# Kernel optimization log

Hardware: AMD Instinct MI355X
Metric: run time of the kernel (lower is better)

## Reference

```python
import jax, jax.numpy as jnp
import numpy as np

B, S, D, H = 1, 2048, 1024, 16
HD = D // H
FF = 4 * D
EPS_LN = 1e-5
EPS_ATTN = 1e-6


def _layernorm(x, g, b):
    mu = jnp.mean(x, axis=-1, keepdims=True)
    var = jnp.mean(jnp.square(x - mu), axis=-1, keepdims=True)
    return (x - mu) * jax.lax.rsqrt(var + EPS_LN) * g + b


def setup_inputs() -> dict:
    key = jax.random.key(0)
    ks = jax.random.split(key, 12)
    w = lambda k, shape: (jax.random.normal(k, shape, jnp.float32) * 0.02)
    return {
        "x": jax.random.normal(ks[0], (B, S, D), jnp.float32),
        "Wq": w(ks[1], (D, D)), "bq": jnp.zeros((D,), jnp.float32),
        "Wk": w(ks[2], (D, D)), "bk": jnp.zeros((D,), jnp.float32),
        "Wv": w(ks[3], (D, D)), "bv": jnp.zeros((D,), jnp.float32),
        "Wo": w(ks[4], (D, D)), "bo": jnp.zeros((D,), jnp.float32),
        "W1": w(ks[5], (FF, D)), "bb1": jnp.zeros((FF,), jnp.float32),
        "W2": w(ks[6], (D, FF)), "bb2": jnp.zeros((D,), jnp.float32),
        "g1": jnp.ones((D,), jnp.float32), "be1": jnp.zeros((D,), jnp.float32),
        "g2": jnp.ones((D,), jnp.float32), "be2": jnp.zeros((D,), jnp.float32),
    }


def reference(x, Wq, bq, Wk, bk, Wv, bv, Wo, bo, W1, bb1, W2, bb2, g1, be1, g2, be2):
    # --- pre-norm causal linear attention ---
    h = _layernorm(x, g1, be1)                     # (B,S,D)
    def heads(t):
        return t.reshape(B, S, H, HD).transpose(0, 2, 1, 3)  # (B,H,S,hd)
    q = heads(h @ Wq.T + bq)
    k = heads(h @ Wk.T + bk)
    v = heads(h @ Wv.T + bv)
    # feature map phi(x) = elu(x) + 1 (strictly positive)
    q = jax.nn.elu(q) + 1.0
    k = jax.nn.elu(k) + 1.0
    # causal cumulative state: S_t = sum_{i<=t} k_i v_i^T ; z_t = sum_{i<=t} k_i
    kv = jnp.cumsum(jnp.einsum("bhsd,bhse->bhsde", k, v), axis=2)  # (B,H,S,hd,hd)
    z = jnp.cumsum(k, axis=2)                                       # (B,H,S,hd)
    num = jnp.einsum("bhsd,bhsde->bhse", q, kv)                    # (B,H,S,hd)
    den = jnp.einsum("bhsd,bhsd->bhs", q, z) + EPS_ATTN
    attn = (num / den[..., None]).transpose(0, 2, 1, 3).reshape(B, S, D)
    attn = attn @ Wo.T + bo
    x = x + attn
    # --- FFN (GELU exact, matching torch nn.GELU default) ---
    h2 = _layernorm(x, g2, be2)
    ff = jax.nn.gelu(h2 @ W1.T + bb1, approximate=False) @ W2.T + bb2
    return x + ff
```

## Files before the change

### kernel.cpp

```cpp
#include <hip/hip_runtime.h>
#include <hip/hip_bf16.h>
#include <math.h>

constexpr int S  = 2048;
constexpr int D  = 1024;
constexpr int H  = 16;
constexpr int HD = 64;
constexpr int FF = 4096;
constexpr int NC  = 32;
constexpr int CHK = 64;
constexpr int QS  = 3 * D;

typedef __attribute__((ext_vector_type(8))) short bf16x8;
typedef __attribute__((ext_vector_type(4))) float f32x4;

__device__ inline unsigned short f2bf(float f) {
    unsigned int u = __float_as_uint(f);
    u = (u + 0x7FFFu + ((u >> 16) & 1u)) >> 16;
    return (unsigned short)u;
}

constexpr int DD4 = D * D / 4;
constexpr int FD4 = FF * D / 4;
constexpr int CVT_TOTAL4 = 4 * DD4 + 2 * FD4;

__global__ __launch_bounds__(256) void cvt6(const float* __restrict__ Wq,
                                            const float* __restrict__ Wk,
                                            const float* __restrict__ Wv,
                                            const float* __restrict__ Wo,
                                            const float* __restrict__ W1,
                                            const float* __restrict__ W2,
                                            unsigned short* __restrict__ Wqkvb,
                                            unsigned short* __restrict__ Wob,
                                            unsigned short* __restrict__ W1b,
                                            unsigned short* __restrict__ W2b) {
    int i = blockIdx.x * 256 + threadIdx.x;
    if (i >= CVT_TOTAL4) return;
    const float* s;
    unsigned short* dp;
    if (i < DD4)                 { s = Wq + (size_t)i * 4;               dp = Wqkvb + (size_t)i * 4; }
    else if (i < 2 * DD4)        { s = Wk + (size_t)(i - DD4) * 4;       dp = Wqkvb + (size_t)i * 4; }
    else if (i < 3 * DD4)        { s = Wv + (size_t)(i - 2 * DD4) * 4;   dp = Wqkvb + (size_t)i * 4; }
    else if (i < 4 * DD4)        { s = Wo + (size_t)(i - 3 * DD4) * 4;   dp = Wob + (size_t)(i - 3 * DD4) * 4; }
    else if (i < 4 * DD4 + FD4)  { s = W1 + (size_t)(i - 4 * DD4) * 4;   dp = W1b + (size_t)(i - 4 * DD4) * 4; }
    else                         { s = W2 + (size_t)(i - 4 * DD4 - FD4) * 4; dp = W2b + (size_t)(i - 4 * DD4 - FD4) * 4; }
    float4 v = *(const float4*)s;
    ushort4 o = { f2bf(v.x), f2bf(v.y), f2bf(v.z), f2bf(v.w) };
    *(ushort4*)dp = o;
}

__global__ __launch_bounds__(256) void layernorm_bf16(const float* __restrict__ x,
                                                      const float* __restrict__ g,
                                                      const float* __restrict__ b,
                                                      unsigned short* __restrict__ out) {
    const int row = blockIdx.x, tid = threadIdx.x;
    float4 v = ((const float4*)(x + (size_t)row * D))[tid];
    float s  = v.x + v.y + v.z + v.w;
    float ss = v.x*v.x + v.y*v.y + v.z*v.z + v.w*v.w;
    #pragma unroll
    for (int off = 32; off > 0; off >>= 1) {
        s  += __shfl_down(s, off);
        ss += __shfl_down(ss, off);
    }
    __shared__ float sw[4], ssw[4];
    if ((tid & 63) == 0) { sw[tid >> 6] = s; ssw[tid >> 6] = ss; }
    __syncthreads();
    s  = sw[0] + sw[1] + sw[2] + sw[3];
    ss = ssw[0] + ssw[1] + ssw[2] + ssw[3];
    const float mu = s * (1.0f / D);
    const float rs = rsqrtf(ss * (1.0f / D) - mu * mu + 1e-5f);
    float4 gv = ((const float4*)g)[tid];
    float4 bv = ((const float4*)b)[tid];
    ushort4 o = { f2bf((v.x - mu) * rs * gv.x + bv.x),
                  f2bf((v.y - mu) * rs * gv.y + bv.y),
                  f2bf((v.z - mu) * rs * gv.z + bv.z),
                  f2bf((v.w - mu) * rs * gv.w + bv.w) };
    ((ushort4*)(out + (size_t)row * D))[tid] = o;
}

template <int KS>
__global__ __launch_bounds__(256) void reduce_ln(const float* __restrict__ part,
                                                 const float* __restrict__ bias,
                                                 const float* __restrict__ res,
                                                 float* __restrict__ x2,
                                                 const float* __restrict__ g,
                                                 const float* __restrict__ b,
                                                 unsigned short* __restrict__ out) {
    const int row = blockIdx.x, tid = threadIdx.x;
    const size_t i4 = (size_t)row * 256 + tid;
    float4 a = ((const float4*)part)[i4];
    #pragma unroll
    for (int z = 1; z < KS; ++z) {
        float4 p = ((const float4*)part)[(size_t)z * S * 256 + i4];
        a.x += p.x; a.y += p.y; a.z += p.z; a.w += p.w;
    }
    float4 bi = ((const float4*)bias)[tid];
    float4 r  = ((const float4*)res)[i4];
    a.x += bi.x + r.x; a.y += bi.y + r.y; a.z += bi.z + r.z; a.w += bi.w + r.w;
    ((float4*)x2)[i4] = a;
    float s  = a.x + a.y + a.z + a.w;
    float ss = a.x*a.x + a.y*a.y + a.z*a.z + a.w*a.w;
    #pragma unroll
    for (int off = 32; off > 0; off >>= 1) {
        s  += __shfl_down(s, off);
        ss += __shfl_down(ss, off);
    }
    __shared__ float sw[4], ssw[4];
    if ((tid & 63) == 0) { sw[tid >> 6] = s; ssw[tid >> 6] = ss; }
    __syncthreads();
    s  = sw[0] + sw[1] + sw[2] + sw[3];
    ss = ssw[0] + ssw[1] + ssw[2] + ssw[3];
    const float mu = s * (1.0f / D);
    const float rs = rsqrtf(ss * (1.0f / D) - mu * mu + 1e-5f);
    float4 gv = ((const float4*)g)[tid];
    float4 bv = ((const float4*)b)[tid];
    ushort4 o = { f2bf((a.x - mu) * rs * gv.x + bv.x),
                  f2bf((a.y - mu) * rs * gv.y + bv.y),
                  f2bf((a.z - mu) * rs * gv.z + bv.z),
                  f2bf((a.w - mu) * rs * gv.w + bv.w) };
    ((ushort4*)(out + (size_t)row * D))[tid] = o;
}

template <int KS>
__global__ __launch_bounds__(256) void reduce_bias_res(const float* __restrict__ part,
                                                       const float* __restrict__ bias,
                                                       const float* __restrict__ res,
                                                       float* __restrict__ out,
                                                       int N4, int total4) {
    int i = blockIdx.x * 256 + threadIdx.x;
    if (i >= total4) return;
    float4 a = ((const float4*)part)[i];
    #pragma unroll
    for (int z = 1; z < KS; ++z) {
        float4 p = ((const float4*)part)[(size_t)z * total4 + i];
        a.x += p.x; a.y += p.y; a.z += p.z; a.w += p.w;
    }
    float4 b = ((const float4*)bias)[i % N4];
    float4 r = ((const float4*)res)[i];
    a.x += b.x + r.x; a.y += b.y + r.y; a.z += b.z + r.z; a.w += b.w + r.w;
    ((float4*)out)[i] = a;
}

enum { EPI_F32 = 0, EPI_QKV = 1, EPI_GELU_BF16 = 2, EPI_PART = 3 };

template <int EPI>
__global__ __launch_bounds__(256, 2) void gemm_bt(const unsigned short* __restrict__ A,
                                                  const unsigned short* __restrict__ W,
                                                  const float* __restrict__ bias,
                                                  const float* __restrict__ bias2,
                                                  const float* __restrict__ bias3,
                                                  void* __restrict__ outp,
                                                  int M, int N, int K, int kSplit) {
    __shared__ unsigned short As[2][128 * 64];
    __shared__ unsigned short Bs[2][128 * 64];
    const int tid  = threadIdx.x;
    const int tileM = blockIdx.x * 128;
    const int tileN = blockIdx.y * 128;
    const int w    = tid >> 6, lane = tid & 63;
    const int wm   = (w >> 1) * 64, wn = (w & 1) * 64;
    const int lr   = lane & 15, lk = lane >> 4;
    const int sw   = (lr >> 1) & 7;
    const int kLen   = K / kSplit;
    const int kStart = blockIdx.z * kLen;
    const int kEnd   = kStart + kLen;

    f32x4 acc[4][4];
    #pragma unroll
    for (int i = 0; i < 4; ++i)
        #pragma unroll
        for (int j = 0; j < 4; ++j) acc[i][j] = (f32x4)(0.0f);

    auto stage = [&](int buf, int k0) {
        #pragma unroll
        for (int p = 0; p < 4; ++p) {
            const int c   = p * 256 + tid;
            const int row = c >> 3;
            const int kc  = (c & 7) ^ ((row >> 1) & 7);
            __builtin_amdgcn_global_load_lds(
                (const __attribute__((address_space(1))) unsigned int*)
                    (A + (size_t)(tileM + row) * K + k0 + kc * 8),
                (__attribute__((address_space(3))) unsigned int*)&As[buf][c * 8],
                16, 0, 0);
            __builtin_amdgcn_global_load_lds(
                (const __attribute__((address_space(1))) unsigned int*)
                    (W + (size_t)(tileN + row) * K + k0 + kc * 8),
                (__attribute__((address_space(3))) unsigned int*)&Bs[buf][c * 8],
                16, 0, 0);
        }
    };

    stage(0, kStart);
    __syncthreads();
    int buf = 0;
    for (int k0 = kStart; k0 < kEnd; k0 += 64) {
        if (k0 + 64 < kEnd) stage(buf ^ 1, k0 + 64);
        #pragma unroll
        for (int kk = 0; kk < 2; ++kk) {
            bf16x8 af[4], bfv[4];
            #pragma unroll
            for (int i = 0; i < 4; ++i) {
                const int row = wm + i * 16 + lr;
                af[i] = *(const bf16x8*)&As[buf][row * 64 + ((((kk << 2) | lk) ^ sw) << 3)];
            }
            #pragma unroll
            for (int j = 0; j < 4; ++j) {
                const int row = wn + j * 16 + lr;
                bfv[j] = *(const bf16x8*)&Bs[buf][row * 64 + ((((kk << 2) | lk) ^ sw) << 3)];
            }
            #pragma unroll
            for (int i = 0; i < 4; ++i)
                #pragma unroll
                for (int j = 0; j < 4; ++j)
                    acc[i][j] = __builtin_amdgcn_mfma_f32_16x16x32_bf16(af[i], bfv[j], acc[i][j], 0, 0, 0);
        }
        __syncthreads();
        buf ^= 1;
    }

    #pragma unroll
    for (int i = 0; i < 4; ++i) {
        const int rbase = tileM + wm + i * 16 + lk * 4;
        #pragma unroll
        for (int j = 0; j < 4; ++j) {
            const int col = tileN + wn + j * 16 + lr;
            #pragma unroll
            for (int r = 0; r < 4; ++r) {
                const int row = rbase + r;
                const size_t off = (size_t)row * N + col;
                float v = acc[i][j][r];
                if constexpr (EPI == EPI_PART) {
                    ((float*)outp)[(size_t)blockIdx.z * (size_t)M * (size_t)N + off] = v;
                } else if constexpr (EPI == EPI_QKV) {
                    float bc = (col < D) ? bias[col] : ((col < 2 * D) ? bias2[col - D] : bias3[col - 2 * D]);
                    v += bc;
                    if (col < 2 * D) v = v > 0.0f ? v + 1.0f : __expf(v);
                    ((float*)outp)[off] = v;
                } else if constexpr (EPI == EPI_GELU_BF16) {
                    v += bias[col];
                    float gl = 0.5f * v * (1.0f + erff(v * 0.70710678118654752f));
                    ((unsigned short*)outp)[off] = f2bf(gl);
                } else {
                    v += bias[col];
                    ((float*)outp)[off] = v;
                }
            }
        }
    }
}

__global__ __launch_bounds__(256) void attn_chunk_sums(const float* __restrict__ qkv,
                                                       float* __restrict__ KVc,
                                                       float* __restrict__ Zc) {
    const int c = blockIdx.x, h = blockIdx.y, tid = threadIdx.x;
    __shared__ float Kc[CHK * HD], Vc[CHK * HD];
    const int s0 = c * CHK;
    #pragma unroll
    for (int p = 0; p < 4; ++p) {
        int cc = p * 256 + tid;
        int t = cc >> 4, dp = (cc & 15) * 4;
        *(float4*)&Kc[t * HD + dp] = *(const float4*)(qkv + (size_t)(s0 + t) * QS + D     + h * HD + dp);
        *(float4*)&Vc[t * HD + dp] = *(const float4*)(qkv + (size_t)(s0 + t) * QS + 2 * D + h * HD + dp);
    }
    __syncthreads();
    const int d = tid >> 2, e0 = (tid & 3) * 16;
    float acc[16];
    #pragma unroll
    for (int j = 0; j < 16; ++j) acc[j] = 0.0f;
    float zacc = 0.0f;
    for (int t = 0; t < CHK; ++t) {
        float kv = Kc[t * HD + d];
        zacc += kv;
        #pragma unroll
        for (int j = 0; j < 16; ++j) acc[j] += kv * Vc[t * HD + e0 + j];
    }
    float* op = KVc + ((size_t)(h * NC + c) * HD + d) * HD + e0;
    #pragma unroll
    for (int j = 0; j < 16; ++j) op[j] = acc[j];
    if ((tid & 3) == 0) Zc[(size_t)(h * NC + c) * HD + d] = zacc;
}

__global__ __launch_bounds__(256) void attn_prefix(float* __restrict__ KVc,
                                                   float* __restrict__ Zc) {
    const int h = blockIdx.y;
    const int elem = blockIdx.x * 256 + threadIdx.x;
    size_t base = (size_t)h * NC * (HD * HD) + elem;
    float run = 0.0f;
    for (int c = 0; c < NC; ++c) {
        float t = KVc[base + (size_t)c * (HD * HD)];
        KVc[base + (size_t)c * (HD * HD)] = run;
        run += t;
    }
    if (blockIdx.x == 0 && threadIdx.x < HD) {
        size_t zb = (size_t)h * NC * HD + threadIdx.x;
        float zr = 0.0f;
        for (int c = 0; c < NC; ++c) {
            float t = Zc[zb + (size_t)c * HD];
            Zc[zb + (size_t)c * HD] = zr;
            zr += t;
        }
    }
}

__global__ __launch_bounds__(256) void attn_out(const float* __restrict__ qkv,
                                                const float* __restrict__ KVpre,
                                                const float* __restrict__ Zpre,
                                                unsigned short* __restrict__ attn) {
    const int c = blockIdx.x, h = blockIdx.y, tid = threadIdx.x;
    __shared__ float Qc[CHK * HD], KVs[CHK * HD], Pre[HD * HD], Sc[CHK * CHK];
    __shared__ float zp[HD], den[CHK];
    const int s0 = c * CHK;
    #pragma unroll
    for (int p = 0; p < 4; ++p) {
        int cc = p * 256 + tid;
        int t = cc >> 4, dp = (cc & 15) * 4;
        *(float4*)&Qc[t * HD + dp]  = *(const float4*)(qkv + (size_t)(s0 + t) * QS +     h * HD + dp);
        *(float4*)&KVs[t * HD + dp] = *(const float4*)(qkv + (size_t)(s0 + t) * QS + D + h * HD + dp);
        ((float4*)Pre)[cc] = *(const float4*)(KVpre + (size_t)(h * NC + c) * (HD * HD) + cc * 4);
    }
    if (tid < HD) zp[tid] = Zpre[(size_t)(h * NC + c) * HD + tid];
    __syncthreads();

    const int tt = tid >> 2, i0 = (tid & 3) * 16;
    for (int i = i0; i < i0 + 16; ++i) {
        float sv = 0.0f;
        for (int d2 = 0; d2 < HD; ++d2) sv += Qc[tt * HD + d2] * KVs[i * HD + d2];
        Sc[tt * CHK + i] = (i <= tt) ? sv : 0.0f;
    }
    __syncthreads();

    if (tid < CHK) {
        float dv = 1e-6f;
        for (int d2 = 0; d2 < HD; ++d2) dv += Qc[tid * HD + d2] * zp[d2];
        for (int i = 0; i < CHK; ++i) dv += Sc[tid * CHK + i];
        den[tid] = dv;
    }
    #pragma unroll
    for (int p = 0; p < 4; ++p) {
        int cc = p * 256 + tid;
        int t = cc >> 4, dp = (cc & 15) * 4;
        *(float4*)&KVs[t * HD + dp] = *(const float4*)(qkv + (size_t)(s0 + t) * QS + 2 * D + h * HD + dp);
    }
    __syncthreads();

    float o[16];
    #pragma unroll
    for (int j = 0; j < 16; ++j) o[j] = 0.0f;
    for (int d2 = 0; d2 < HD; ++d2) {
        float qv = Qc[tt * HD + d2];
        float sv = Sc[tt * CHK + d2];
        #pragma unroll
        for (int j = 0; j < 16; ++j)
            o[j] += qv * Pre[d2 * HD + i0 + j] + sv * KVs[d2 * HD + i0 + j];
    }
    const float inv = 1.0f / den[tt];
    unsigned short* op = attn + (size_t)(s0 + tt) * D + h * HD + i0;
    #pragma unroll
    for (int j0 = 0; j0 < 16; j0 += 4) {
        ushort4 ov = { f2bf(o[j0] * inv), f2bf(o[j0 + 1] * inv),
                       f2bf(o[j0 + 2] * inv), f2bf(o[j0 + 3] * inv) };
        *(ushort4*)(op + j0) = ov;
    }
}

extern "C" void kernel_launch(void* const* d_in, const int* in_sizes, int n_in,
                              void* d_out, int out_size, void* d_ws, size_t ws_size,
                              hipStream_t stream) {
    const float* x   = (const float*)d_in[0];
    const float* Wq  = (const float*)d_in[1];
    const float* bq  = (const float*)d_in[2];
    const float* Wk  = (const float*)d_in[3];
    const float* bk  = (const float*)d_in[4];
    const float* Wv  = (const float*)d_in[5];
    const float* bv  = (const float*)d_in[6];
    const float* Wo  = (const float*)d_in[7];
    const float* bo  = (const float*)d_in[8];
    const float* W1  = (const float*)d_in[9];
    const float* b1  = (const float*)d_in[10];
    const float* W2  = (const float*)d_in[11];
    const float* b2  = (const float*)d_in[12];
    const float* g1  = (const float*)d_in[13];
    const float* be1 = (const float*)d_in[14];
    const float* g2  = (const float*)d_in[15];
    const float* be2 = (const float*)d_in[16];
    float* out = (float*)d_out;

    char* wsp = (char*)d_ws;
    auto alloc = [&](size_t bytes) {
        char* p = wsp;
        wsp += (bytes + 255) & ~(size_t)255;
        return p;
    };
    unsigned short* h1   = (unsigned short*)alloc((size_t)S * D * 2);
    unsigned short* attn = (unsigned short*)alloc((size_t)S * D * 2);
    unsigned short* gbuf = (unsigned short*)alloc((size_t)S * FF * 2);
    float* x2   = (float*)alloc((size_t)S * D * 4);
    unsigned short* Wqkvb = (unsigned short*)alloc((size_t)3 * D * D * 2);
    unsigned short* Wob   = (unsigned short*)alloc((size_t)D * D * 2);
    unsigned short* W1b   = (unsigned short*)alloc((size_t)FF * D * 2);
    unsigned short* W2b   = (unsigned short*)alloc((size_t)D * FF * 2);
    float* KVc  = (float*)alloc((size_t)H * NC * HD * HD * 4);
    float* Zc   = (float*)alloc((size_t)H * NC * HD * 4);
    char* uni = (char*)alloc((size_t)32 * 1024 * 1024);
    float* qkv   = (float*)uni;
    float* parts = (float*)uni;

    cvt6<<<(CVT_TOTAL4 + 255) / 256, 256, 0, stream>>>(Wq, Wk, Wv, Wo, W1, W2,
                                                       Wqkvb, Wob, W1b, W2b);

    layernorm_bf16<<<S, 256, 0, stream>>>(x, g1, be1, h1);

    gemm_bt<EPI_QKV><<<dim3(S / 128, 3 * D / 128, 1), 256, 0, stream>>>(
        h1, Wqkvb, bq, bk, bv, qkv, S, 3 * D, D, 1);

    attn_chunk_sums<<<dim3(NC, H), 256, 0, stream>>>(qkv, KVc, Zc);
    attn_prefix<<<dim3(16, H), 256, 0, stream>>>(KVc, Zc);
    attn_out<<<dim3(NC, H), 256, 0, stream>>>(qkv, KVc, Zc, attn);

    gemm_bt<EPI_PART><<<dim3(S / 128, D / 128, 4), 256, 0, stream>>>(
        attn, Wob, nullptr, nullptr, nullptr, parts, S, D, D, 4);
    reduce_ln<4><<<S, 256, 0, stream>>>(parts, bo, x, x2, g2, be2, h1);

    gemm_bt<EPI_GELU_BF16><<<dim3(S / 128, FF / 128, 1), 256, 0, stream>>>(
        h1, W1b, b1, nullptr, nullptr, gbuf, S, FF, D, 1);

    gemm_bt<EPI_PART><<<dim3(S / 128, D / 128, 4), 256, 0, stream>>>(
        gbuf, W2b, nullptr, nullptr, nullptr, parts, S, D, FF, 4);
    reduce_bias_res<4><<<(S * D / 4 + 255) / 256, 256, 0, stream>>>(
        parts, b2, x2, out, D / 4, S * D / 4);
}
```

Measured before the change: 280.3 us.

## Replace split-K partial buffers with atomic accumulation into pre-initialized outputs

The split-K GEMMs for the output projection and the second FFN layer now atomically add their partial results into destination buffers instead of writing four partial slabs and reducing them in separate kernels. The destinations are pre-initialized with residual plus bias: x2 inside a merged prep kernel that also does the weight conversion and the first layernorm, and out inside the second layernorm kernel. This removes the partial-buffer writes and reads and two reduction passes, and folds two early launches into one. In exchange it adds float atomic traffic with nondeterministic summation order, and the epilogue's scalar atomics may be slower than plain stores.

```diff
diff --git a/kernel.cpp b/kernel.cpp
--- a/kernel.cpp
+++ b/kernel.cpp
@@ -23,8 +23,10 @@
 constexpr int DD4 = D * D / 4;
 constexpr int FD4 = FF * D / 4;
 constexpr int CVT_TOTAL4 = 4 * DD4 + 2 * FD4;
-
-__global__ __launch_bounds__(256) void cvt6(const float* __restrict__ Wq,
+constexpr int NB_CVT  = CVT_TOTAL4 / 256;
+constexpr int NB_INIT = S * D / 4 / 256;
+
+__global__ __launch_bounds__(256) void prep(const float* __restrict__ Wq,
                                             const float* __restrict__ Wk,
                                             const float* __restrict__ Wv,
                                             const float* __restrict__ Wo,
@@ -33,71 +35,72 @@
                                             unsigned short* __restrict__ Wqkvb,
                                             unsigned short* __restrict__ Wob,
                                             unsigned short* __restrict__ W1b,
-                                            unsigned short* __restrict__ W2b) {
-    int i = blockIdx.x * 256 + threadIdx.x;
-    if (i >= CVT_TOTAL4) return;
-    const float* s;
-    unsigned short* dp;
-    if (i < DD4)                 { s = Wq + (size_t)i * 4;               dp = Wqkvb + (size_t)i * 4; }
-    else if (i < 2 * DD4)        { s = Wk + (size_t)(i - DD4) * 4;       dp = Wqkvb + (size_t)i * 4; }
-    else if (i < 3 * DD4)        { s = Wv + (size_t)(i - 2 * DD4) * 4;   dp = Wqkvb + (size_t)i * 4; }
-    else if (i < 4 * DD4)        { s = Wo + (size_t)(i - 3 * DD4) * 4;   dp = Wob + (size_t)(i - 3 * DD4) * 4; }
-    else if (i < 4 * DD4 + FD4)  { s = W1 + (size_t)(i - 4 * DD4) * 4;   dp = W1b + (size_t)(i - 4 * DD4) * 4; }
-    else                         { s = W2 + (size_t)(i - 4 * DD4 - FD4) * 4; dp = W2b + (size_t)(i - 4 * DD4 - FD4) * 4; }
-    float4 v = *(const float4*)s;
-    ushort4 o = { f2bf(v.x), f2bf(v.y), f2bf(v.z), f2bf(v.w) };
-    *(ushort4*)dp = o;
-}
-
-__global__ __launch_bounds__(256) void layernorm_bf16(const float* __restrict__ x,
-                                                      const float* __restrict__ g,
-                                                      const float* __restrict__ b,
-                                                      unsigned short* __restrict__ out) {
-    const int row = blockIdx.x, tid = threadIdx.x;
-    float4 v = ((const float4*)(x + (size_t)row * D))[tid];
-    float s  = v.x + v.y + v.z + v.w;
-    float ss = v.x*v.x + v.y*v.y + v.z*v.z + v.w*v.w;
-    #pragma unroll
-    for (int off = 32; off > 0; off >>= 1) {
-        s  += __shfl_down(s, off);
-        ss += __shfl_down(ss, off);
-    }
-    __shared__ float sw[4], ssw[4];
-    if ((tid & 63) == 0) { sw[tid >> 6] = s; ssw[tid >> 6] = ss; }
-    __syncthreads();
-    s  = sw[0] + sw[1] + sw[2] + sw[3];
-    ss = ssw[0] + ssw[1] + ssw[2] + ssw[3];
-    const float mu = s * (1.0f / D);
-    const float rs = rsqrtf(ss * (1.0f / D) - mu * mu + 1e-5f);
-    float4 gv = ((const float4*)g)[tid];
-    float4 bv = ((const float4*)b)[tid];
-    ushort4 o = { f2bf((v.x - mu) * rs * gv.x + bv.x),
-                  f2bf((v.y - mu) * rs * gv.y + bv.y),
-                  f2bf((v.z - mu) * rs * gv.z + bv.z),
-                  f2bf((v.w - mu) * rs * gv.w + bv.w) };
-    ((ushort4*)(out + (size_t)row * D))[tid] = o;
-}
-
-template <int KS>
-__global__ __launch_bounds__(256) void reduce_ln(const float* __restrict__ part,
-                                                 const float* __restrict__ bias,
-                                                 const float* __restrict__ res,
-                                                 float* __restrict__ x2,
-                                                 const float* __restrict__ g,
-                                                 const float* __restrict__ b,
-                                                 unsigned short* __restrict__ out) {
+                                            unsigned short* __restrict__ W2b,
+                                            const float* __restrict__ x,
+                                            const float* __restrict__ g1,
+                                            const float* __restrict__ be1,
+                                            unsigned short* __restrict__ h1,
+                                            const float* __restrict__ bo,
+                                            float* __restrict__ x2) {
+    const int b = blockIdx.x, tid = threadIdx.x;
+    if (b < NB_CVT) {
+        int i = b * 256 + tid;
+        const float* s;
+        unsigned short* dp;
+        if (i < DD4)                 { s = Wq + (size_t)i * 4;               dp = Wqkvb + (size_t)i * 4; }
+        else if (i < 2 * DD4)        { s = Wk + (size_t)(i - DD4) * 4;       dp = Wqkvb + (size_t)i * 4; }
+        else if (i < 3 * DD4)        { s = Wv + (size_t)(i - 2 * DD4) * 4;   dp = Wqkvb + (size_t)i * 4; }
+        else if (i < 4 * DD4)        { s = Wo + (size_t)(i - 3 * DD4) * 4;   dp = Wob + (size_t)(i - 3 * DD4) * 4; }
+        else if (i < 4 * DD4 + FD4)  { s = W1 + (size_t)(i - 4 * DD4) * 4;   dp = W1b + (size_t)(i - 4 * DD4) * 4; }
+        else                         { s = W2 + (size_t)(i - 4 * DD4 - FD4) * 4; dp = W2b + (size_t)(i - 4 * DD4 - FD4) * 4; }
+        float4 v = *(const float4*)s;
+        ushort4 o = { f2bf(v.x), f2bf(v.y), f2bf(v.z), f2bf(v.w) };
+        *(ushort4*)dp = o;
+    } else if (b < NB_CVT + S) {
+        const int row = b - NB_CVT;
+        float4 v = ((const float4*)(x + (size_t)row * D))[tid];
+        float s  = v.x + v.y + v.z + v.w;
+        float ss = v.x*v.x + v.y*v.y + v.z*v.z + v.w*v.w;
+        #pragma unroll
+        for (int off = 32; off > 0; off >>= 1) {
+            s  += __shfl_down(s, off);
+            ss += __shfl_down(ss, off);
+        }
+        __shared__ float sw[4], ssw[4];
+        if ((tid & 63) == 0) { sw[tid >> 6] = s; ssw[tid >> 6] = ss; }
+        __syncthreads();
+        s  = sw[0] + sw[1] + sw[2] + sw[3];
+        ss = ssw[0] + ssw[1] + ssw[2] + ssw[3];
+        const float mu = s * (1.0f / D);
+        const float rs = rsqrtf(ss * (1.0f / D) - mu * mu + 1e-5f);
+        float4 gv = ((const float4*)g1)[tid];
+        float4 bv = ((const float4*)be1)[tid];
+        ushort4 o = { f2bf((v.x - mu) * rs * gv.x + bv.x),
+                      f2bf((v.y - mu) * rs * gv.y + bv.y),
+                      f2bf((v.z - mu) * rs * gv.z + bv.z),
+                      f2bf((v.w - mu) * rs * gv.w + bv.w) };
+        ((ushort4*)(h1 + (size_t)row * D))[tid] = o;
+    } else {
+        const int i = (b - NB_CVT - S) * 256 + tid;
+        float4 v = ((const float4*)x)[i];
+        float4 bb = ((const float4*)bo)[i & 255];
+        v.x += bb.x; v.y += bb.y; v.z += bb.z; v.w += bb.w;
+        ((float4*)x2)[i] = v;
+    }
+}
+
+__global__ __launch_bounds__(256) void ln2_init(const float* __restrict__ x2,
+                                                const float* __restrict__ g,
+                                                const float* __restrict__ b,
+                                                const float* __restrict__ b2,
+                                                unsigned short* __restrict__ hout,
+                                                float* __restrict__ out) {
     const int row = blockIdx.x, tid = threadIdx.x;
     const size_t i4 = (size_t)row * 256 + tid;
-    float4 a = ((const float4*)part)[i4];
-    #pragma unroll
-    for (int z = 1; z < KS; ++z) {
-        float4 p = ((const float4*)part)[(size_t)z * S * 256 + i4];
-        a.x += p.x; a.y += p.y; a.z += p.z; a.w += p.w;
-    }
-    float4 bi = ((const float4*)bias)[tid];
-    float4 r  = ((const float4*)res)[i4];
-    a.x += bi.x + r.x; a.y += bi.y + r.y; a.z += bi.z + r.z; a.w += bi.w + r.w;
-    ((float4*)x2)[i4] = a;
+    float4 a = ((const float4*)x2)[i4];
+    float4 b2v = ((const float4*)b2)[tid];
+    float4 ov = { a.x + b2v.x, a.y + b2v.y, a.z + b2v.z, a.w + b2v.w };
+    ((float4*)out)[i4] = ov;
     float s  = a.x + a.y + a.z + a.w;
     float ss = a.x*a.x + a.y*a.y + a.z*a.z + a.w*a.w;
     #pragma unroll
@@ -118,30 +121,10 @@
                   f2bf((a.y - mu) * rs * gv.y + bv.y),
                   f2bf((a.z - mu) * rs * gv.z + bv.z),
                   f2bf((a.w - mu) * rs * gv.w + bv.w) };
-    ((ushort4*)(out + (size_t)row * D))[tid] = o;
-}
-
-template <int KS>
-__global__ __launch_bounds__(256) void reduce_bias_res(const float* __restrict__ part,
-                                                       const float* __restrict__ bias,
-                                                       const float* __restrict__ res,
-                                                       float* __restrict__ out,
-                                                       int N4, int total4) {
-    int i = blockIdx.x * 256 + threadIdx.x;
-    if (i >= total4) return;
-    float4 a = ((const float4*)part)[i];
-    #pragma unroll
-    for (int z = 1; z < KS; ++z) {
-        float4 p = ((const float4*)part)[(size_t)z * total4 + i];
-        a.x += p.x; a.y += p.y; a.z += p.z; a.w += p.w;
-    }
-    float4 b = ((const float4*)bias)[i % N4];
-    float4 r = ((const float4*)res)[i];
-    a.x += b.x + r.x; a.y += b.y + r.y; a.z += b.z + r.z; a.w += b.w + r.w;
-    ((float4*)out)[i] = a;
-}
-
-enum { EPI_F32 = 0, EPI_QKV = 1, EPI_GELU_BF16 = 2, EPI_PART = 3 };
+    ((ushort4*)(hout + (size_t)row * D))[tid] = o;
+}
+
+enum { EPI_F32 = 0, EPI_QKV = 1, EPI_GELU_BF16 = 2, EPI_ATOM = 3 };
 
 template <int EPI>
 __global__ __launch_bounds__(256, 2) void gemm_bt(const unsigned short* __restrict__ A,
@@ -228,8 +211,8 @@
                 const int row = rbase + r;
                 const size_t off = (size_t)row * N + col;
                 float v = acc[i][j][r];
-                if constexpr (EPI == EPI_PART) {
-                    ((float*)outp)[(size_t)blockIdx.z * (size_t)M * (size_t)N + off] = v;
+                if constexpr (EPI == EPI_ATOM) {
+                    atomicAdd(&((float*)outp)[off], v);
                 } else if constexpr (EPI == EPI_QKV) {
                     float bc = (col < D) ? bias[col] : ((col < 2 * D) ? bias2[col - D] : bias3[col - 2 * D]);
                     v += bc;
@@ -400,14 +383,11 @@
     unsigned short* W2b   = (unsigned short*)alloc((size_t)D * FF * 2);
     float* KVc  = (float*)alloc((size_t)H * NC * HD * HD * 4);
     float* Zc   = (float*)alloc((size_t)H * NC * HD * 4);
-    char* uni = (char*)alloc((size_t)32 * 1024 * 1024);
-    float* qkv   = (float*)uni;
-    float* parts = (float*)uni;
-
-    cvt6<<<(CVT_TOTAL4 + 255) / 256, 256, 0, stream>>>(Wq, Wk, Wv, Wo, W1, W2,
-                                                       Wqkvb, Wob, W1b, W2b);
-
-    layernorm_bf16<<<S, 256, 0, stream>>>(x, g1, be1, h1);
+    float* qkv  = (float*)alloc((size_t)S * QS * 4);
+
+    prep<<<NB_CVT + S + NB_INIT, 256, 0, stream>>>(Wq, Wk, Wv, Wo, W1, W2,
+                                                   Wqkvb, Wob, W1b, W2b,
+                                                   x, g1, be1, h1, bo, x2);
 
     gemm_bt<EPI_QKV><<<dim3(S / 128, 3 * D / 128, 1), 256, 0, stream>>>(
         h1, Wqkvb, bq, bk, bv, qkv, S, 3 * D, D, 1);
@@ -416,15 +396,14 @@
     attn_prefix<<<dim3(16, H), 256, 0, stream>>>(KVc, Zc);
     attn_out<<<dim3(NC, H), 256, 0, stream>>>(qkv, KVc, Zc, attn);
 
-    gemm_bt<EPI_PART><<<dim3(S / 128, D / 128, 4), 256, 0, stream>>>(
-        attn, Wob, nullptr, nullptr, nullptr, parts, S, D, D, 4);
-    reduce_ln<4><<<S, 256, 0, stream>>>(parts, bo, x, x2, g2, be2, h1);
+    gemm_bt<EPI_ATOM><<<dim3(S / 128, D / 128, 4), 256, 0, stream>>>(
+        attn, Wob, nullptr, nullptr, nullptr, x2, S, D, D, 4);
+
+    ln2_init<<<S, 256, 0, stream>>>(x2, g2, be2, b2, h1, out);
 
     gemm_bt<EPI_GELU_BF16><<<dim3(S / 128, FF / 128, 1), 256, 0, stream>>>(
         h1, W1b, b1, nullptr, nullptr, gbuf, S, FF, D, 1);
 
-    gemm_bt<EPI_PART><<<dim3(S / 128, D / 128, 4), 256, 0, stream>>>(
-        gbuf, W2b, nullptr, nullptr, nullptr, parts, S, D, FF, 4);
-    reduce_bias_res<4><<<(S * D / 4 + 255) / 256, 256, 0, stream>>>(
-        parts, b2, x2, out, D / 4, S * D / 4);
-}
+    gemm_bt<EPI_ATOM><<<dim3(S / 128, D / 128, 4), 256, 0, stream>>>(
+        gbuf, W2b, nullptr, nullptr, nullptr, out, S, D, FF, 4);
+}
```

After: 307.1 us. +9.5%, slower.

## Shrink GEMM M-tile to 64, merge weight conversion with first layernorm

Applied to the files above, without the earlier changes.

The GEMM tile changes from 128x128 to 64x128, which halves the A staging and accumulators and raises the occupancy hint to 3 blocks per CU. Grids and split-K factors are adjusted to match: the Wo GEMM goes from 4 to 2 splits with a matching reduce, and the W2 GEMM keeps 4 splits. The weight bf16 conversion and the first layernorm are merged into one launch to save a kernel launch. The aim is more blocks to fill the many CUs and less partial-sum traffic, at the cost of lower per-block arithmetic intensity, since more B tiles must be reloaded.

```diff
diff --git a/kernel.cpp b/kernel.cpp
--- a/kernel.cpp
+++ b/kernel.cpp
@@ -23,8 +23,9 @@
 constexpr int DD4 = D * D / 4;
 constexpr int FD4 = FF * D / 4;
 constexpr int CVT_TOTAL4 = 4 * DD4 + 2 * FD4;
-
-__global__ __launch_bounds__(256) void cvt6(const float* __restrict__ Wq,
+constexpr int NB_CVT  = CVT_TOTAL4 / 256;
+
+__global__ __launch_bounds__(256) void prep(const float* __restrict__ Wq,
                                             const float* __restrict__ Wk,
                                             const float* __restrict__ Wv,
                                             const float* __restrict__ Wo,
@@ -33,49 +34,50 @@
                                             unsigned short* __restrict__ Wqkvb,
                                             unsigned short* __restrict__ Wob,
                                             unsigned short* __restrict__ W1b,
-                                            unsigned short* __restrict__ W2b) {
-    int i = blockIdx.x * 256 + threadIdx.x;
-    if (i >= CVT_TOTAL4) return;
-    const float* s;
-    unsigned short* dp;
-    if (i < DD4)                 { s = Wq + (size_t)i * 4;               dp = Wqkvb + (size_t)i * 4; }
-    else if (i < 2 * DD4)        { s = Wk + (size_t)(i - DD4) * 4;       dp = Wqkvb + (size_t)i * 4; }
-    else if (i < 3 * DD4)        { s = Wv + (size_t)(i - 2 * DD4) * 4;   dp = Wqkvb + (size_t)i * 4; }
-    else if (i < 4 * DD4)        { s = Wo + (size_t)(i - 3 * DD4) * 4;   dp = Wob + (size_t)(i - 3 * DD4) * 4; }
-    else if (i < 4 * DD4 + FD4)  { s = W1 + (size_t)(i - 4 * DD4) * 4;   dp = W1b + (size_t)(i - 4 * DD4) * 4; }
-    else                         { s = W2 + (size_t)(i - 4 * DD4 - FD4) * 4; dp = W2b + (size_t)(i - 4 * DD4 - FD4) * 4; }
-    float4 v = *(const float4*)s;
-    ushort4 o = { f2bf(v.x), f2bf(v.y), f2bf(v.z), f2bf(v.w) };
-    *(ushort4*)dp = o;
-}
-
-__global__ __launch_bounds__(256) void layernorm_bf16(const float* __restrict__ x,
-                                                      const float* __restrict__ g,
-                                                      const float* __restrict__ b,
-                                                      unsigned short* __restrict__ out) {
-    const int row = blockIdx.x, tid = threadIdx.x;
-    float4 v = ((const float4*)(x + (size_t)row * D))[tid];
-    float s  = v.x + v.y + v.z + v.w;
-    float ss = v.x*v.x + v.y*v.y + v.z*v.z + v.w*v.w;
-    #pragma unroll
-    for (int off = 32; off > 0; off >>= 1) {
-        s  += __shfl_down(s, off);
-        ss += __shfl_down(ss, off);
-    }
-    __shared__ float sw[4], ssw[4];
-    if ((tid & 63) == 0) { sw[tid >> 6] = s; ssw[tid >> 6] = ss; }
-    __syncthreads();
-    s  = sw[0] + sw[1] + sw[2] + sw[3];
-    ss = ssw[0] + ssw[1] + ssw[2] + ssw[3];
-    const float mu = s * (1.0f / D);
-    const float rs = rsqrtf(ss * (1.0f / D) - mu * mu + 1e-5f);
-    float4 gv = ((const float4*)g)[tid];
-    float4 bv = ((const float4*)b)[tid];
-    ushort4 o = { f2bf((v.x - mu) * rs * gv.x + bv.x),
-                  f2bf((v.y - mu) * rs * gv.y + bv.y),
-                  f2bf((v.z - mu) * rs * gv.z + bv.z),
-                  f2bf((v.w - mu) * rs * gv.w + bv.w) };
-    ((ushort4*)(out + (size_t)row * D))[tid] = o;
+                                            unsigned short* __restrict__ W2b,
+                                            const float* __restrict__ x,
+                                            const float* __restrict__ g1,
+                                            const float* __restrict__ be1,
+                                            unsigned short* __restrict__ h1) {
+    const int b = blockIdx.x, tid = threadIdx.x;
+    if (b < NB_CVT) {
+        int i = b * 256 + tid;
+        const float* s;
+        unsigned short* dp;
+        if (i < DD4)                 { s = Wq + (size_t)i * 4;               dp = Wqkvb + (size_t)i * 4; }
+        else if (i < 2 * DD4)        { s = Wk + (size_t)(i - DD4) * 4;       dp = Wqkvb + (size_t)i * 4; }
+        else if (i < 3 * DD4)        { s = Wv + (size_t)(i - 2 * DD4) * 4;   dp = Wqkvb + (size_t)i * 4; }
+        else if (i < 4 * DD4)        { s = Wo + (size_t)(i - 3 * DD4) * 4;   dp = Wob + (size_t)(i - 3 * DD4) * 4; }
+        else if (i < 4 * DD4 + FD4)  { s = W1 + (size_t)(i - 4 * DD4) * 4;   dp = W1b + (size_t)(i - 4 * DD4) * 4; }
+        else                         { s = W2 + (size_t)(i - 4 * DD4 - FD4) * 4; dp = W2b + (size_t)(i - 4 * DD4 - FD4) * 4; }
+        float4 v = *(const float4*)s;
+        ushort4 o = { f2bf(v.x), f2bf(v.y), f2bf(v.z), f2bf(v.w) };
+        *(ushort4*)dp = o;
+    } else {
+        const int row = b - NB_CVT;
+        float4 v = ((const float4*)(x + (size_t)row * D))[tid];
+        float s  = v.x + v.y + v.z + v.w;
+        float ss = v.x*v.x + v.y*v.y + v.z*v.z + v.w*v.w;
+        #pragma unroll
+        for (int off = 32; off > 0; off >>= 1) {
+            s  += __shfl_down(s, off);
+            ss += __shfl_down(ss, off);
+        }
+        __shared__ float sw[4], ssw[4];
+        if ((tid & 63) == 0) { sw[tid >> 6] = s; ssw[tid >> 6] = ss; }
+        __syncthreads();
+        s  = sw[0] + sw[1] + sw[2] + sw[3];
+        ss = ssw[0] + ssw[1] + ssw[2] + ssw[3];
+        const float mu = s * (1.0f / D);
+        const float rs = rsqrtf(ss * (1.0f / D) - mu * mu + 1e-5f);
+        float4 gv = ((const float4*)g1)[tid];
+        float4 bv = ((const float4*)be1)[tid];
+        ushort4 o = { f2bf((v.x - mu) * rs * gv.x + bv.x),
+                      f2bf((v.y - mu) * rs * gv.y + bv.y),
+                      f2bf((v.z - mu) * rs * gv.z + bv.z),
+                      f2bf((v.w - mu) * rs * gv.w + bv.w) };
+        ((ushort4*)(h1 + (size_t)row * D))[tid] = o;
+    }
 }
 
 template <int KS>
@@ -144,35 +146,35 @@
 enum { EPI_F32 = 0, EPI_QKV = 1, EPI_GELU_BF16 = 2, EPI_PART = 3 };
 
 template <int EPI>
-__global__ __launch_bounds__(256, 2) void gemm_bt(const unsigned short* __restrict__ A,
+__global__ __launch_bounds__(256, 3) void gemm_bt(const unsigned short* __restrict__ A,
                                                   const unsigned short* __restrict__ W,
                                                   const float* __restrict__ bias,
                                                   const float* __restrict__ bias2,
                                                   const float* __restrict__ bias3,
                                                   void* __restrict__ outp,
                                                   int M, int N, int K, int kSplit) {
-    __shared__ unsigned short As[2][128 * 64];
+    __shared__ unsigned short As[2][64 * 64];
     __shared__ unsigned short Bs[2][128 * 64];
     const int tid  = threadIdx.x;
-    const int tileM = blockIdx.x * 128;
+    const int tileM = blockIdx.x * 64;
     const int tileN = blockIdx.y * 128;
     const int w    = tid >> 6, lane = tid & 63;
-    const int wm   = (w >> 1) * 64, wn = (w & 1) * 64;
+    const int wm   = (w >> 1) * 32, wn = (w & 1) * 64;
     const int lr   = lane & 15, lk = lane >> 4;
     const int sw   = (lr >> 1) & 7;
     const int kLen   = K / kSplit;
     const int kStart = blockIdx.z * kLen;
     const int kEnd   = kStart + kLen;
 
-    f32x4 acc[4][4];
-    #pragma unroll
-    for (int i = 0; i < 4; ++i)
+    f32x4 acc[2][4];
+    #pragma unroll
+    for (int i = 0; i < 2; ++i)
         #pragma unroll
         for (int j = 0; j < 4; ++j) acc[i][j] = (f32x4)(0.0f);
 
     auto stage = [&](int buf, int k0) {
         #pragma unroll
-        for (int p = 0; p < 4; ++p) {
+        for (int p = 0; p < 2; ++p) {
             const int c   = p * 256 + tid;
             const int row = c >> 3;
             const int kc  = (c & 7) ^ ((row >> 1) & 7);
@@ -181,6 +183,12 @@
                     (A + (size_t)(tileM + row) * K + k0 + kc * 8),
                 (__attribute__((address_space(3))) unsigned int*)&As[buf][c * 8],
                 16, 0, 0);
+        }
+        #pragma unroll
+        for (int p = 0; p < 4; ++p) {
+            const int c   = p * 256 + tid;
+            const int row = c >> 3;
+            const int kc  = (c & 7) ^ ((row >> 1) & 7);
             __builtin_amdgcn_global_load_lds(
                 (const __attribute__((address_space(1))) unsigned int*)
                     (W + (size_t)(tileN + row) * K + k0 + kc * 8),
@@ -196,9 +204,9 @@
         if (k0 + 64 < kEnd) stage(buf ^ 1, k0 + 64);
         #pragma unroll
         for (int kk = 0; kk < 2; ++kk) {
-            bf16x8 af[4], bfv[4];
+            bf16x8 af[2], bfv[4];
             #pragma unroll
-            for (int i = 0; i < 4; ++i) {
+            for (int i = 0; i < 2; ++i) {
                 const int row = wm + i * 16 + lr;
                 af[i] = *(const bf16x8*)&As[buf][row * 64 + ((((kk << 2) | lk) ^ sw) << 3)];
             }
@@ -208,7 +216,7 @@
                 bfv[j] = *(const bf16x8*)&Bs[buf][row * 64 + ((((kk << 2) | lk) ^ sw) << 3)];
             }
             #pragma unroll
-            for (int i = 0; i < 4; ++i)
+            for (int i = 0; i < 2; ++i)
                 #pragma unroll
                 for (int j = 0; j < 4; ++j)
                     acc[i][j] = __builtin_amdgcn_mfma_f32_16x16x32_bf16(af[i], bfv[j], acc[i][j], 0, 0, 0);
@@ -218,7 +226,7 @@
     }
 
     #pragma unroll
-    for (int i = 0; i < 4; ++i) {
+    for (int i = 0; i < 2; ++i) {
         const int rbase = tileM + wm + i * 16 + lk * 4;
         #pragma unroll
         for (int j = 0; j < 4; ++j) {
@@ -404,26 +412,25 @@
     float* qkv   = (float*)uni;
     float* parts = (float*)uni;
 
-    cvt6<<<(CVT_TOTAL4 + 255) / 256, 256, 0, stream>>>(Wq, Wk, Wv, Wo, W1, W2,
-                                                       Wqkvb, Wob, W1b, W2b);
-
-    layernorm_bf16<<<S, 256, 0, stream>>>(x, g1, be1, h1);
-
-    gemm_bt<EPI_QKV><<<dim3(S / 128, 3 * D / 128, 1), 256, 0, stream>>>(
+    prep<<<NB_CVT + S, 256, 0, stream>>>(Wq, Wk, Wv, Wo, W1, W2,
+                                         Wqkvb, Wob, W1b, W2b,
+                                         x, g1, be1, h1);
+
+    gemm_bt<EPI_QKV><<<dim3(S / 64, 3 * D / 128, 1), 256, 0, stream>>>(
         h1, Wqkvb, bq, bk, bv, qkv, S, 3 * D, D, 1);
 
     attn_chunk_sums<<<dim3(NC, H), 256, 0, stream>>>(qkv, KVc, Zc);
     attn_prefix<<<dim3(16, H), 256, 0, stream>>>(KVc, Zc);
     attn_out<<<dim3(NC, H), 256, 0, stream>>>(qkv, KVc, Zc, attn);
 
-    gemm_bt<EPI_PART><<<dim3(S / 128, D / 128, 4), 256, 0, stream>>>(
-        attn, Wob, nullptr, nullptr, nullptr, parts, S, D, D, 4);
-    reduce_ln<4><<<S, 256, 0, stream>>>(parts, bo, x, x2, g2, be2, h1);
-
-    gemm_bt<EPI_GELU_BF16><<<dim3(S / 128, FF / 128, 1), 256, 0, stream>>>(
+    gemm_bt<EPI_PART><<<dim3(S / 64, D / 128, 2), 256, 0, stream>>>(
+        attn, Wob, nullptr, nullptr, nullptr, parts, S, D, D, 2);
+    reduce_ln<2><<<S, 256, 0, stream>>>(parts, bo, x, x2, g2, be2, h1);
+
+    gemm_bt<EPI_GELU_BF16><<<dim3(S / 64, FF / 128, 1), 256, 0, stream>>>(
         h1, W1b, b1, nullptr, nullptr, gbuf, S, FF, D, 1);
 
-    gemm_bt<EPI_PART><<<dim3(S / 128, D / 128, 4), 256, 0, stream>>>(
+    gemm_bt<EPI_PART><<<dim3(S / 64, D / 128, 4), 256, 0, stream>>>(
         gbuf, W2b, nullptr, nullptr, nullptr, parts, S, D, FF, 4);
     reduce_bias_res<4><<<(S * D / 4 + 255) / 256, 256, 0, stream>>>(
         parts, b2, x2, out, D / 4, S * D / 4);
```

Result: slower. 288.6 us (+2.9%).

## Store QKV activations as bf16 and merge weight conversion with first layernorm

Applied to the files above, without the earlier changes.

The QKV GEMM epilogue now writes bf16 instead of fp32, and the attention kernels read bf16 and widen it to fp32 in shared memory. This halves the QKV intermediate traffic. The weight-cast kernel and the first layernorm are fused into one launch that uses separate block ranges, which removes one kernel launch. Q, K and V lose precision when rounded to bf16 before the linear-attention cumulative sums.

```diff
diff --git a/kernel.cpp b/kernel.cpp
--- a/kernel.cpp
+++ b/kernel.cpp
@@ -19,12 +19,16 @@
     u = (u + 0x7FFFu + ((u >> 16) & 1u)) >> 16;
     return (unsigned short)u;
 }
+__device__ inline float bf2f(unsigned short u) {
+    return __uint_as_float(((unsigned int)u) << 16);
+}
 
 constexpr int DD4 = D * D / 4;
 constexpr int FD4 = FF * D / 4;
 constexpr int CVT_TOTAL4 = 4 * DD4 + 2 * FD4;
-
-__global__ __launch_bounds__(256) void cvt6(const float* __restrict__ Wq,
+constexpr int NB_CVT  = CVT_TOTAL4 / 256;
+
+__global__ __launch_bounds__(256) void prep(const float* __restrict__ Wq,
                                             const float* __restrict__ Wk,
                                             const float* __restrict__ Wv,
                                             const float* __restrict__ Wo,
@@ -33,49 +37,50 @@
                                             unsigned short* __restrict__ Wqkvb,
                                             unsigned short* __restrict__ Wob,
                                             unsigned short* __restrict__ W1b,
-                                            unsigned short* __restrict__ W2b) {
-    int i = blockIdx.x * 256 + threadIdx.x;
-    if (i >= CVT_TOTAL4) return;
-    const float* s;
-    unsigned short* dp;
-    if (i < DD4)                 { s = Wq + (size_t)i * 4;               dp = Wqkvb + (size_t)i * 4; }
-    else if (i < 2 * DD4)        { s = Wk + (size_t)(i - DD4) * 4;       dp = Wqkvb + (size_t)i * 4; }
-    else if (i < 3 * DD4)        { s = Wv + (size_t)(i - 2 * DD4) * 4;   dp = Wqkvb + (size_t)i * 4; }
-    else if (i < 4 * DD4)        { s = Wo + (size_t)(i - 3 * DD4) * 4;   dp = Wob + (size_t)(i - 3 * DD4) * 4; }
-    else if (i < 4 * DD4 + FD4)  { s = W1 + (size_t)(i - 4 * DD4) * 4;   dp = W1b + (size_t)(i - 4 * DD4) * 4; }
-    else                         { s = W2 + (size_t)(i - 4 * DD4 - FD4) * 4; dp = W2b + (size_t)(i - 4 * DD4 - FD4) * 4; }
-    float4 v = *(const float4*)s;
-    ushort4 o = { f2bf(v.x), f2bf(v.y), f2bf(v.z), f2bf(v.w) };
-    *(ushort4*)dp = o;
-}
-
-__global__ __launch_bounds__(256) void layernorm_bf16(const float* __restrict__ x,
-                                                      const float* __restrict__ g,
-                                                      const float* __restrict__ b,
-                                                      unsigned short* __restrict__ out) {
-    const int row = blockIdx.x, tid = threadIdx.x;
-    float4 v = ((const float4*)(x + (size_t)row * D))[tid];
-    float s  = v.x + v.y + v.z + v.w;
-    float ss = v.x*v.x + v.y*v.y + v.z*v.z + v.w*v.w;
-    #pragma unroll
-    for (int off = 32; off > 0; off >>= 1) {
-        s  += __shfl_down(s, off);
-        ss += __shfl_down(ss, off);
-    }
-    __shared__ float sw[4], ssw[4];
-    if ((tid & 63) == 0) { sw[tid >> 6] = s; ssw[tid >> 6] = ss; }
-    __syncthreads();
-    s  = sw[0] + sw[1] + sw[2] + sw[3];
-    ss = ssw[0] + ssw[1] + ssw[2] + ssw[3];
-    const float mu = s * (1.0f / D);
-    const float rs = rsqrtf(ss * (1.0f / D) - mu * mu + 1e-5f);
-    float4 gv = ((const float4*)g)[tid];
-    float4 bv = ((const float4*)b)[tid];
-    ushort4 o = { f2bf((v.x - mu) * rs * gv.x + bv.x),
-                  f2bf((v.y - mu) * rs * gv.y + bv.y),
-                  f2bf((v.z - mu) * rs * gv.z + bv.z),
-                  f2bf((v.w - mu) * rs * gv.w + bv.w) };
-    ((ushort4*)(out + (size_t)row * D))[tid] = o;
+                                            unsigned short* __restrict__ W2b,
+                                            const float* __restrict__ x,
+                                            const float* __restrict__ g1,
+                                            const float* __restrict__ be1,
+                                            unsigned short* __restrict__ h1) {
+    const int b = blockIdx.x, tid = threadIdx.x;
+    if (b < NB_CVT) {
+        int i = b * 256 + tid;
+        const float* s;
+        unsigned short* dp;
+        if (i < DD4)                 { s = Wq + (size_t)i * 4;               dp = Wqkvb + (size_t)i * 4; }
+        else if (i < 2 * DD4)        { s = Wk + (size_t)(i - DD4) * 4;       dp = Wqkvb + (size_t)i * 4; }
+        else if (i < 3 * DD4)        { s = Wv + (size_t)(i - 2 * DD4) * 4;   dp = Wqkvb + (size_t)i * 4; }
+        else if (i < 4 * DD4)        { s = Wo + (size_t)(i - 3 * DD4) * 4;   dp = Wob + (size_t)(i - 3 * DD4) * 4; }
+        else if (i < 4 * DD4 + FD4)  { s = W1 + (size_t)(i - 4 * DD4) * 4;   dp = W1b + (size_t)(i - 4 * DD4) * 4; }
+        else                         { s = W2 + (size_t)(i - 4 * DD4 - FD4) * 4; dp = W2b + (size_t)(i - 4 * DD4 - FD4) * 4; }
+        float4 v = *(const float4*)s;
+        ushort4 o = { f2bf(v.x), f2bf(v.y), f2bf(v.z), f2bf(v.w) };
+        *(ushort4*)dp = o;
+    } else {
+        const int row = b - NB_CVT;
+        float4 v = ((const float4*)(x + (size_t)row * D))[tid];
+        float s  = v.x + v.y + v.z + v.w;
+        float ss = v.x*v.x + v.y*v.y + v.z*v.z + v.w*v.w;
+        #pragma unroll
+        for (int off = 32; off > 0; off >>= 1) {
+            s  += __shfl_down(s, off);
+            ss += __shfl_down(ss, off);
+        }
+        __shared__ float sw[4], ssw[4];
+        if ((tid & 63) == 0) { sw[tid >> 6] = s; ssw[tid >> 6] = ss; }
+        __syncthreads();
+        s  = sw[0] + sw[1] + sw[2] + sw[3];
+        ss = ssw[0] + ssw[1] + ssw[2] + ssw[3];
+        const float mu = s * (1.0f / D);
+        const float rs = rsqrtf(ss * (1.0f / D) - mu * mu + 1e-5f);
+        float4 gv = ((const float4*)g1)[tid];
+        float4 bv = ((const float4*)be1)[tid];
+        ushort4 o = { f2bf((v.x - mu) * rs * gv.x + bv.x),
+                      f2bf((v.y - mu) * rs * gv.y + bv.y),
+                      f2bf((v.z - mu) * rs * gv.z + bv.z),
+                      f2bf((v.w - mu) * rs * gv.w + bv.w) };
+        ((ushort4*)(h1 + (size_t)row * D))[tid] = o;
+    }
 }
 
 template <int KS>
@@ -141,7 +146,7 @@
     ((float4*)out)[i] = a;
 }
 
-enum { EPI_F32 = 0, EPI_QKV = 1, EPI_GELU_BF16 = 2, EPI_PART = 3 };
+enum { EPI_F32 = 0, EPI_QKV_BF16 = 1, EPI_GELU_BF16 = 2, EPI_PART = 3 };
 
 template <int EPI>
 __global__ __launch_bounds__(256, 2) void gemm_bt(const unsigned short* __restrict__ A,
@@ -230,11 +235,11 @@
                 float v = acc[i][j][r];
                 if constexpr (EPI == EPI_PART) {
                     ((float*)outp)[(size_t)blockIdx.z * (size_t)M * (size_t)N + off] = v;
-                } else if constexpr (EPI == EPI_QKV) {
+                } else if constexpr (EPI == EPI_QKV_BF16) {
                     float bc = (col < D) ? bias[col] : ((col < 2 * D) ? bias2[col - D] : bias3[col - 2 * D]);
                     v += bc;
                     if (col < 2 * D) v = v > 0.0f ? v + 1.0f : __expf(v);
-                    ((float*)outp)[off] = v;
+                    ((unsigned short*)outp)[off] = f2bf(v);
                 } else if constexpr (EPI == EPI_GELU_BF16) {
                     v += bias[col];
                     float gl = 0.5f * v * (1.0f + erff(v * 0.70710678118654752f));
@@ -248,7 +253,7 @@
     }
 }
 
-__global__ __launch_bounds__(256) void attn_chunk_sums(const float* __restrict__ qkv,
+__global__ __launch_bounds__(256) void attn_chunk_sums(const unsigned short* __restrict__ qkv,
                                                        float* __restrict__ KVc,
                                                        float* __restrict__ Zc) {
     const int c = blockIdx.x, h = blockIdx.y, tid = threadIdx.x;
@@ -258,8 +263,10 @@
     for (int p = 0; p < 4; ++p) {
         int cc = p * 256 + tid;
         int t = cc >> 4, dp = (cc & 15) * 4;
-        *(float4*)&Kc[t * HD + dp] = *(const float4*)(qkv + (size_t)(s0 + t) * QS + D     + h * HD + dp);
-        *(float4*)&Vc[t * HD + dp] = *(const float4*)(qkv + (size_t)(s0 + t) * QS + 2 * D + h * HD + dp);
+        ushort4 kv4 = *(const ushort4*)(qkv + (size_t)(s0 + t) * QS + D     + h * HD + dp);
+        ushort4 vv4 = *(const ushort4*)(qkv + (size_t)(s0 + t) * QS + 2 * D + h * HD + dp);
+        *(float4*)&Kc[t * HD + dp] = { bf2f(kv4.x), bf2f(kv4.y), bf2f(kv4.z), bf2f(kv4.w) };
+        *(float4*)&Vc[t * HD + dp] = { bf2f(vv4.x), bf2f(vv4.y), bf2f(vv4.z), bf2f(vv4.w) };
     }
     __syncthreads();
     const int d = tid >> 2, e0 = (tid & 3) * 16;
@@ -301,7 +308,7 @@
     }
 }
 
-__global__ __launch_bounds__(256) void attn_out(const float* __restrict__ qkv,
+__global__ __launch_bounds__(256) void attn_out(const unsigned short* __restrict__ qkv,
                                                 const float* __restrict__ KVpre,
                                                 const float* __restrict__ Zpre,
                                                 unsigned short* __restrict__ attn) {
@@ -313,8 +320,10 @@
     for (int p = 0; p < 4; ++p) {
         int cc = p * 256 + tid;
         int t = cc >> 4, dp = (cc & 15) * 4;
-        *(float4*)&Qc[t * HD + dp]  = *(const float4*)(qkv + (size_t)(s0 + t) * QS +     h * HD + dp);
-        *(float4*)&KVs[t * HD + dp] = *(const float4*)(qkv + (size_t)(s0 + t) * QS + D + h * HD + dp);
+        ushort4 q4 = *(const ushort4*)(qkv + (size_t)(s0 + t) * QS +     h * HD + dp);
+        ushort4 k4 = *(const ushort4*)(qkv + (size_t)(s0 + t) * QS + D + h * HD + dp);
+        *(float4*)&Qc[t * HD + dp]  = { bf2f(q4.x), bf2f(q4.y), bf2f(q4.z), bf2f(q4.w) };
+        *(float4*)&KVs[t * HD + dp] = { bf2f(k4.x), bf2f(k4.y), bf2f(k4.z), bf2f(k4.w) };
         ((float4*)Pre)[cc] = *(const float4*)(KVpre + (size_t)(h * NC + c) * (HD * HD) + cc * 4);
     }
     if (tid < HD) zp[tid] = Zpre[(size_t)(h * NC + c) * HD + tid];
@@ -338,7 +347,8 @@
     for (int p = 0; p < 4; ++p) {
         int cc = p * 256 + tid;
         int t = cc >> 4, dp = (cc & 15) * 4;
-        *(float4*)&KVs[t * HD + dp] = *(const float4*)(qkv + (size_t)(s0 + t) * QS + 2 * D + h * HD + dp);
+        ushort4 v4 = *(const ushort4*)(qkv + (size_t)(s0 + t) * QS + 2 * D + h * HD + dp);
+        *(float4*)&KVs[t * HD + dp] = { bf2f(v4.x), bf2f(v4.y), bf2f(v4.z), bf2f(v4.w) };
     }
     __syncthreads();
 
@@ -401,15 +411,14 @@
     float* KVc  = (float*)alloc((size_t)H * NC * HD * HD * 4);
     float* Zc   = (float*)alloc((size_t)H * NC * HD * 4);
     char* uni = (char*)alloc((size_t)32 * 1024 * 1024);
-    float* qkv   = (float*)uni;
-    float* parts = (float*)uni;
-
-    cvt6<<<(CVT_TOTAL4 + 255) / 256, 256, 0, stream>>>(Wq, Wk, Wv, Wo, W1, W2,
-                                                       Wqkvb, Wob, W1b, W2b);
-
-    layernorm_bf16<<<S, 256, 0, stream>>>(x, g1, be1, h1);
-
-    gemm_bt<EPI_QKV><<<dim3(S / 128, 3 * D / 128, 1), 256, 0, stream>>>(
+    unsigned short* qkv = (unsigned short*)uni;
+    float* parts        = (float*)uni;
+
+    prep<<<NB_CVT + S, 256, 0, stream>>>(Wq, Wk, Wv, Wo, W1, W2,
+                                         Wqkvb, Wob, W1b, W2b,
+                                         x, g1, be1, h1);
+
+    gemm_bt<EPI_QKV_BF16><<<dim3(S / 128, 3 * D / 128, 1), 256, 0, stream>>>(
         h1, Wqkvb, bq, bk, bv, qkv, S, 3 * D, D, 1);
 
     attn_chunk_sums<<<dim3(NC, H), 256, 0, stream>>>(qkv, KVc, Zc);
```

Result: no change. 280.6 us (+0.1%).
